# Kernel optimization log

Measured on AMD Instinct MI355X. Metric: run time of the kernel, lower is better.

## Reference

```python
import jax, jax.numpy as jnp
import numpy as np

BN_EPS = 1e-5


def setup_inputs() -> dict:
    key = jax.random.key(0)
    ks = jax.random.split(key, 12)
    B, D, N, M, H = 8, 3, 20000, 1024, 1024
    x = jax.random.normal(ks[0], (B, D, N), dtype=jnp.float32)
    # random basis points inside a unit ball (as bps.generate_random_basis)
    dirs = jax.random.normal(ks[1], (M, D), dtype=jnp.float32)
    dirs = dirs / jnp.linalg.norm(dirs, axis=1, keepdims=True)
    r = jax.random.uniform(ks[2], (M, 1), dtype=jnp.float32) ** (1.0 / 3.0)
    basis = dirs * r
    return {
        "x": x,
        "basis": basis,
        "bn1_g": jax.random.uniform(ks[3], (M,), dtype=jnp.float32) + 0.5,
        "bn1_b": jax.random.normal(ks[4], (M,), dtype=jnp.float32) * 0.1,
        "bn1_rm": jax.random.normal(ks[5], (M,), dtype=jnp.float32) * 0.1,
        "bn1_rv": jax.random.uniform(ks[6], (M,), dtype=jnp.float32) + 0.5,
        "w1": jax.random.normal(ks[7], (H, M), dtype=jnp.float32) * (1.0 / np.sqrt(M)),
        "b1": jnp.zeros((H,), dtype=jnp.float32),
        "bn2_g": jax.random.uniform(ks[8], (H,), dtype=jnp.float32) + 0.5,
        "bn2_b": jax.random.normal(ks[9], (H,), dtype=jnp.float32) * 0.1,
        "bn2_rm": jax.random.normal(ks[10], (H,), dtype=jnp.float32) * 0.1,
        "bn2_rv": jax.random.uniform(ks[11], (H,), dtype=jnp.float32) + 0.5,
        "w2": jax.random.normal(jax.random.fold_in(key, 99), (1, H), dtype=jnp.float32) * (1.0 / np.sqrt(H)),
        "b2": jnp.zeros((1,), dtype=jnp.float32),
    }


def _bps_encode(x, basis):
    # x: [B, 3, N]; basis: [M, 3] -> sqrt(min_n ||p_n - b_m||^2): [B, M]
    pts = jnp.transpose(x, (0, 2, 1))                      # [B, N, 3]
    x2 = jnp.sum(pts * pts, axis=-1)                       # [B, N]
    b2 = jnp.sum(basis * basis, axis=-1)                   # [M]
    cross = jnp.einsum('bnd,md->bnm', pts, basis)          # [B, N, M]
    dist2 = x2[:, :, None] + b2[None, None, :] - 2.0 * cross
    dist2 = jnp.clip(dist2, 0.0, None)
    return jnp.sqrt(jnp.min(dist2, axis=1))                # [B, M]


def _bn_eval(f, g, b, rm, rv):
    return (f - rm) * (g / jnp.sqrt(rv + BN_EPS)) + b


def reference(x, basis, bn1_g, bn1_b, bn1_rm, bn1_rv, w1, b1,
              bn2_g, bn2_b, bn2_rm, bn2_rv, w2, b2):
    f = _bps_encode(x, basis)                              # [B, M]
    f = _bn_eval(f, bn1_g, bn1_b, bn1_rm, bn1_rv)
    f = f @ w1.T + b1                                      # [B, 1024]
    f = jax.nn.relu(f)
    f = _bn_eval(f, bn2_g, bn2_b, bn2_rm, bn2_rv)
    # Dropout(p=0.8) is identity in eval mode
    out = f @ w2.T + b2                                    # [B, 1]
    return out
```

## Files before the change

### kernel.cpp

```cpp
#include <hip/hip_runtime.h>
#include <hip/hip_bf16.h>
#include <math.h>

#define B 8
#define NPTS 20000
#define M 1024
#define H 1024
#define BN_EPS 1e-5f

#define BPS_BLOCK 256
#define BPS_CHUNK 250
#define BPS_NCHUNK 80
#define L1_MCHUNK 128

__global__ __launch_bounds__(256) void init_kernel(unsigned int* __restrict__ fmin,
                                                   float* __restrict__ h,
                                                   const float* __restrict__ b1) {
    int idx = blockIdx.x * 256 + threadIdx.x;
    if (idx < B * M) {
        fmin[idx] = 0x7F800000u;
    } else {
        int j = idx - B * M;
        h[j] = b1[j & (H - 1)];
    }
}

__global__ __launch_bounds__(256) void bps_kernel(const float* __restrict__ x,
                                                  const float* __restrict__ basis,
                                                  unsigned int* __restrict__ fmin) {
    __shared__ float4 pts[BPS_CHUNK];
    const int chunk = blockIdx.x;
    const int b = blockIdx.y;
    const int tid = threadIdx.x;
    const int n0 = chunk * BPS_CHUNK;
    const float* xb = x + (size_t)b * 3 * NPTS;

    for (int i = tid; i < BPS_CHUNK; i += BPS_BLOCK) {
        float px = xb[n0 + i];
        float py = xb[NPTS + n0 + i];
        float pz = xb[2 * NPTS + n0 + i];
        pts[i] = make_float4(px, py, pz, px * px + py * py + pz * pz);
    }

    float nbx[4], nby[4], nbz[4], bb2[4];
#pragma unroll
    for (int k = 0; k < 4; ++k) {
        int m = tid + k * 256;
        float bx = basis[m * 3 + 0];
        float by = basis[m * 3 + 1];
        float bz = basis[m * 3 + 2];
        nbx[k] = -2.0f * bx;
        nby[k] = -2.0f * by;
        nbz[k] = -2.0f * bz;
        bb2[k] = bx * bx + by * by + bz * bz;
    }
    float acc[4] = {INFINITY, INFINITY, INFINITY, INFINITY};
    __syncthreads();

#pragma unroll 2
    for (int n = 0; n < BPS_CHUNK; n += 2) {
        float4 p0 = pts[n];
        float4 p1 = pts[n + 1];
#pragma unroll
        for (int k = 0; k < 4; ++k) {
            float s0 = p0.w + bb2[k];
            s0 = fmaf(p0.x, nbx[k], s0);
            s0 = fmaf(p0.y, nby[k], s0);
            s0 = fmaf(p0.z, nbz[k], s0);
            float s1 = p1.w + bb2[k];
            s1 = fmaf(p1.x, nbx[k], s1);
            s1 = fmaf(p1.y, nby[k], s1);
            s1 = fmaf(p1.z, nbz[k], s1);
            acc[k] = fminf(acc[k], fminf(s0, s1));
        }
    }

#pragma unroll
    for (int k = 0; k < 4; ++k) {
        float v = fmaxf(acc[k], 0.0f);
        atomicMin(&fmin[b * M + tid + k * 256], __float_as_uint(v));
    }
}

__global__ __launch_bounds__(256) void layer1_kernel(const unsigned int* __restrict__ fmin,
                                                     const float* __restrict__ g1,
                                                     const float* __restrict__ bb1,
                                                     const float* __restrict__ rm1,
                                                     const float* __restrict__ rv1,
                                                     const float* __restrict__ w1,
                                                     float* __restrict__ h) {
    __shared__ float fs[B][L1_MCHUNK];
    const int tid = threadIdx.x;
    const int i = blockIdx.x * 256 + tid;
    const int m0 = blockIdx.y * L1_MCHUNK;

    for (int e = tid; e < B * L1_MCHUNK; e += 256) {
        int bb = e >> 7;
        int ml = e & (L1_MCHUNK - 1);
        int m = m0 + ml;
        float f = sqrtf(__uint_as_float(fmin[bb * M + m]));
        float sc = g1[m] / sqrtf(rv1[m] + BN_EPS);
        fs[bb][ml] = (f - rm1[m]) * sc + bb1[m];
    }
    __syncthreads();

    float acc[B] = {0, 0, 0, 0, 0, 0, 0, 0};
    const float* wrow = w1 + (size_t)i * M + m0;
    for (int ml = 0; ml < L1_MCHUNK; ml += 4) {
        float4 w = *reinterpret_cast<const float4*>(wrow + ml);
#pragma unroll
        for (int bb = 0; bb < B; ++bb) {
            float4 f = *reinterpret_cast<const float4*>(&fs[bb][ml]);
            acc[bb] = fmaf(f.x, w.x, acc[bb]);
            acc[bb] = fmaf(f.y, w.y, acc[bb]);
            acc[bb] = fmaf(f.z, w.z, acc[bb]);
            acc[bb] = fmaf(f.w, w.w, acc[bb]);
        }
    }
#pragma unroll
    for (int bb = 0; bb < B; ++bb) atomicAdd(&h[bb * H + i], acc[bb]);
}

__global__ __launch_bounds__(256) void final_kernel(const float* __restrict__ h,
                                                    const float* __restrict__ g2,
                                                    const float* __restrict__ bb2v,
                                                    const float* __restrict__ rm2,
                                                    const float* __restrict__ rv2,
                                                    const float* __restrict__ w2,
                                                    const float* __restrict__ b2,
                                                    float* __restrict__ out) {
    const int b = blockIdx.x;
    const int tid = threadIdx.x;
    float sum = 0.0f;
    for (int i = tid; i < H; i += 256) {
        float v = fmaxf(h[b * H + i], 0.0f);
        float sc = g2[i] / sqrtf(rv2[i] + BN_EPS);
        v = (v - rm2[i]) * sc + bb2v[i];
        sum += v * w2[i];
    }
#pragma unroll
    for (int off = 32; off > 0; off >>= 1) sum += __shfl_down(sum, off, 64);
    __shared__ float wsum[4];
    if ((tid & 63) == 0) wsum[tid >> 6] = sum;
    __syncthreads();
    if (tid == 0) out[b] = wsum[0] + wsum[1] + wsum[2] + wsum[3] + b2[0];
}

extern "C" void kernel_launch(void* const* d_in, const int* in_sizes, int n_in,
                              void* d_out, int out_size, void* d_ws, size_t ws_size,
                              hipStream_t stream) {
    const float* x      = (const float*)d_in[0];
    const float* basis  = (const float*)d_in[1];
    const float* bn1_g  = (const float*)d_in[2];
    const float* bn1_b  = (const float*)d_in[3];
    const float* bn1_rm = (const float*)d_in[4];
    const float* bn1_rv = (const float*)d_in[5];
    const float* w1     = (const float*)d_in[6];
    const float* b1     = (const float*)d_in[7];
    const float* bn2_g  = (const float*)d_in[8];
    const float* bn2_b  = (const float*)d_in[9];
    const float* bn2_rm = (const float*)d_in[10];
    const float* bn2_rv = (const float*)d_in[11];
    const float* w2     = (const float*)d_in[12];
    const float* b2     = (const float*)d_in[13];
    float* out = (float*)d_out;

    unsigned int* fmin = (unsigned int*)d_ws;
    float* h = (float*)((char*)d_ws + (size_t)B * M * 4);

    init_kernel<<<(2 * B * M) / 256, 256, 0, stream>>>(fmin, h, b1);

    dim3 gB(BPS_NCHUNK, B);
    bps_kernel<<<gB, BPS_BLOCK, 0, stream>>>(x, basis, fmin);

    dim3 gC(H / 256, M / L1_MCHUNK);
    layer1_kernel<<<gC, 256, 0, stream>>>(fmin, bn1_g, bn1_b, bn1_rm, bn1_rv, w1, h);

    final_kernel<<<B, 256, 0, stream>>>(h, bn2_g, bn2_b, bn2_rm, bn2_rv, w2, b2, out);
}
```

Measured before the change: 41.39 us.

## Replace atomics and init kernel with partial-result buffers; pack BPS math as float2

Removes the init kernel and the atomicMin/atomicAdd reductions. BPS and layer1 now write per-chunk partial minima and partial sums to workspace, and the consumer kernels reduce them. The BPS inner loop is rewritten with float2 SoA shared memory and packed FMAs, and the basis-norm add is hoisted out of the loop. Chunk sizes also change to 125x8 BPS blocks and 32-wide layer1 M chunks. The cost is more workspace traffic: a 125-way min read in layer1 and a 32-way sum read in final_kernel, which runs on only 8 blocks.

```diff
diff --git a/kernel.cpp b/kernel.cpp
--- a/kernel.cpp
+++ b/kernel.cpp
@@ -8,38 +8,33 @@
 #define H 1024
 #define BN_EPS 1e-5f
 
-#define BPS_BLOCK 256
-#define BPS_CHUNK 250
-#define BPS_NCHUNK 80
-#define L1_MCHUNK 128
+#define BPS_CHUNK 160
+#define BPS_NCHUNK 125
+#define BPS_PAIRS (BPS_CHUNK / 2)
 
-__global__ __launch_bounds__(256) void init_kernel(unsigned int* __restrict__ fmin,
-                                                   float* __restrict__ h,
-                                                   const float* __restrict__ b1) {
-    int idx = blockIdx.x * 256 + threadIdx.x;
-    if (idx < B * M) {
-        fmin[idx] = 0x7F800000u;
-    } else {
-        int j = idx - B * M;
-        h[j] = b1[j & (H - 1)];
-    }
-}
+#define L1_MCHUNK 32
+#define L1_NMCHUNK (M / L1_MCHUNK)
+
+typedef float f2 __attribute__((ext_vector_type(2)));
 
 __global__ __launch_bounds__(256) void bps_kernel(const float* __restrict__ x,
                                                   const float* __restrict__ basis,
-                                                  unsigned int* __restrict__ fmin) {
-    __shared__ float4 pts[BPS_CHUNK];
+                                                  float* __restrict__ pmin) {
+    __shared__ f2 sx2[BPS_PAIRS], sy2[BPS_PAIRS], sz2[BPS_PAIRS], sw2[BPS_PAIRS];
     const int chunk = blockIdx.x;
     const int b = blockIdx.y;
     const int tid = threadIdx.x;
     const int n0 = chunk * BPS_CHUNK;
     const float* xb = x + (size_t)b * 3 * NPTS;
 
-    for (int i = tid; i < BPS_CHUNK; i += BPS_BLOCK) {
-        float px = xb[n0 + i];
-        float py = xb[NPTS + n0 + i];
-        float pz = xb[2 * NPTS + n0 + i];
-        pts[i] = make_float4(px, py, pz, px * px + py * py + pz * pz);
+    if (tid < BPS_CHUNK) {
+        float px = xb[n0 + tid];
+        float py = xb[NPTS + n0 + tid];
+        float pz = xb[2 * NPTS + n0 + tid];
+        ((float*)sx2)[tid] = px;
+        ((float*)sy2)[tid] = py;
+        ((float*)sz2)[tid] = pz;
+        ((float*)sw2)[tid] = px * px + py * py + pz * pz;
     }
 
     float nbx[4], nby[4], nbz[4], bb2[4];
@@ -58,54 +53,62 @@
     __syncthreads();
 
 #pragma unroll 2
-    for (int n = 0; n < BPS_CHUNK; n += 2) {
-        float4 p0 = pts[n];
-        float4 p1 = pts[n + 1];
+    for (int j = 0; j < BPS_PAIRS; ++j) {
+        f2 X = sx2[j];
+        f2 Y = sy2[j];
+        f2 Z = sz2[j];
+        f2 W = sw2[j];
 #pragma unroll
         for (int k = 0; k < 4; ++k) {
-            float s0 = p0.w + bb2[k];
-            s0 = fmaf(p0.x, nbx[k], s0);
-            s0 = fmaf(p0.y, nby[k], s0);
-            s0 = fmaf(p0.z, nbz[k], s0);
-            float s1 = p1.w + bb2[k];
-            s1 = fmaf(p1.x, nbx[k], s1);
-            s1 = fmaf(p1.y, nby[k], s1);
-            s1 = fmaf(p1.z, nbz[k], s1);
-            acc[k] = fminf(acc[k], fminf(s0, s1));
+            f2 s = W;
+            f2 bx = {nbx[k], nbx[k]};
+            f2 by = {nby[k], nby[k]};
+            f2 bz = {nbz[k], nbz[k]};
+            s = __builtin_elementwise_fma(X, bx, s);
+            s = __builtin_elementwise_fma(Y, by, s);
+            s = __builtin_elementwise_fma(Z, bz, s);
+            acc[k] = fminf(acc[k], fminf(s.x, s.y));
         }
     }
 
 #pragma unroll
     for (int k = 0; k < 4; ++k) {
-        float v = fmaxf(acc[k], 0.0f);
-        atomicMin(&fmin[b * M + tid + k * 256], __float_as_uint(v));
+        float v = fmaxf(acc[k] + bb2[k], 0.0f);
+        pmin[((size_t)chunk * B + b) * M + tid + k * 256] = v;
     }
 }
 
-__global__ __launch_bounds__(256) void layer1_kernel(const unsigned int* __restrict__ fmin,
+__global__ __launch_bounds__(256) void layer1_kernel(const float* __restrict__ pmin,
                                                      const float* __restrict__ g1,
                                                      const float* __restrict__ bb1,
                                                      const float* __restrict__ rm1,
                                                      const float* __restrict__ rv1,
                                                      const float* __restrict__ w1,
-                                                     float* __restrict__ h) {
+                                                     float* __restrict__ hpart) {
     __shared__ float fs[B][L1_MCHUNK];
     const int tid = threadIdx.x;
     const int i = blockIdx.x * 256 + tid;
-    const int m0 = blockIdx.y * L1_MCHUNK;
+    const int mc = blockIdx.y;
+    const int m0 = mc * L1_MCHUNK;
 
-    for (int e = tid; e < B * L1_MCHUNK; e += 256) {
-        int bb = e >> 7;
-        int ml = e & (L1_MCHUNK - 1);
+    {
+        int bb = tid >> 5;
+        int ml = tid & (L1_MCHUNK - 1);
         int m = m0 + ml;
-        float f = sqrtf(__uint_as_float(fmin[bb * M + m]));
-        float sc = g1[m] / sqrtf(rv1[m] + BN_EPS);
+        float v = INFINITY;
+#pragma unroll 5
+        for (int c = 0; c < BPS_NCHUNK; ++c) {
+            v = fminf(v, pmin[((size_t)c * B + bb) * M + m]);
+        }
+        float f = sqrtf(v);
+        float sc = g1[m] * rsqrtf(rv1[m] + BN_EPS);
         fs[bb][ml] = (f - rm1[m]) * sc + bb1[m];
     }
     __syncthreads();
 
     float acc[B] = {0, 0, 0, 0, 0, 0, 0, 0};
     const float* wrow = w1 + (size_t)i * M + m0;
+#pragma unroll
     for (int ml = 0; ml < L1_MCHUNK; ml += 4) {
         float4 w = *reinterpret_cast<const float4*>(wrow + ml);
 #pragma unroll
@@ -118,10 +121,11 @@
         }
     }
 #pragma unroll
-    for (int bb = 0; bb < B; ++bb) atomicAdd(&h[bb * H + i], acc[bb]);
+    for (int bb = 0; bb < B; ++bb) hpart[((size_t)mc * B + bb) * H + i] = acc[bb];
 }
 
-__global__ __launch_bounds__(256) void final_kernel(const float* __restrict__ h,
+__global__ __launch_bounds__(256) void final_kernel(const float* __restrict__ hpart,
+                                                    const float* __restrict__ b1,
                                                     const float* __restrict__ g2,
                                                     const float* __restrict__ bb2v,
                                                     const float* __restrict__ rm2,
@@ -133,8 +137,13 @@
     const int tid = threadIdx.x;
     float sum = 0.0f;
     for (int i = tid; i < H; i += 256) {
-        float v = fmaxf(h[b * H + i], 0.0f);
-        float sc = g2[i] / sqrtf(rv2[i] + BN_EPS);
+        float hs = 0.0f;
+#pragma unroll 8
+        for (int mc = 0; mc < L1_NMCHUNK; ++mc) {
+            hs += hpart[((size_t)mc * B + b) * H + i];
+        }
+        float v = fmaxf(hs + b1[i], 0.0f);
+        float sc = g2[i] * rsqrtf(rv2[i] + BN_EPS);
         v = (v - rm2[i]) * sc + bb2v[i];
         sum += v * w2[i];
     }
@@ -165,16 +174,14 @@
     const float* b2     = (const float*)d_in[13];
     float* out = (float*)d_out;
 
-    unsigned int* fmin = (unsigned int*)d_ws;
-    float* h = (float*)((char*)d_ws + (size_t)B * M * 4);
+    float* pmin  = (float*)d_ws;
+    float* hpart = (float*)((char*)d_ws + (size_t)BPS_NCHUNK * B * M * 4);
 
-    init_kernel<<<(2 * B * M) / 256, 256, 0, stream>>>(fmin, h, b1);
+    dim3 g1g(BPS_NCHUNK, B);
+    bps_kernel<<<g1g, 256, 0, stream>>>(x, basis, pmin);
 
-    dim3 gB(BPS_NCHUNK, B);
-    bps_kernel<<<gB, BPS_BLOCK, 0, stream>>>(x, basis, fmin);
+    dim3 g2g(H / 256, L1_NMCHUNK);
+    layer1_kernel<<<g2g, 256, 0, stream>>>(pmin, bn1_g, bn1_b, bn1_rm, bn1_rv, w1, hpart);
 
-    dim3 gC(H / 256, M / L1_MCHUNK);
-    layer1_kernel<<<gC, 256, 0, stream>>>(fmin, bn1_g, bn1_b, bn1_rm, bn1_rv, w1, h);
-
-    final_kernel<<<B, 256, 0, stream>>>(h, bn2_g, bn2_b, bn2_rm, bn2_rv, w2, b2, out);
+    final_kernel<<<B, 256, 0, stream>>>(hpart, b1, bn2_g, bn2_b, bn2_rm, bn2_rv, w2, b2, out);
 }
```

Result: slower. 55.20 us (+33.4%).
